# Kernel tuning notes

Measured on AMD Instinct MI355X. Metric: run time of the kernel, lower is better.

Reference implementation:

```python
import jax, jax.numpy as jnp
import numpy as np

QW_MAX = 127  # 2**(8-1) - 1


def setup_inputs() -> dict:
    key = jax.random.key(0)
    k1, k2, k3, k4, k5 = jax.random.split(key, 5)
    B, Din, H, Dout = 4096, 1024, 4096, 1024
    x = jax.random.normal(k1, (B, Din), dtype=jnp.float32)
    # float master weights (already transposed, as in quantify_weights: weight.T)
    w1f = jax.random.normal(k2, (Din, H), dtype=jnp.float32) * 0.02
    b1f = jax.random.normal(k3, (H,), dtype=jnp.float32) * 0.02
    w2f = jax.random.normal(k4, (H, Dout), dtype=jnp.float32) * 0.02
    b2f = jax.random.normal(k5, (Dout,), dtype=jnp.float32) * 0.02
    return {"x": x, "w1f": w1f, "b1f": b1f, "w2f": w2f, "b2f": b2f}


def _quantify_pair(w, b):
    # joint max-abs scale over weight and bias (matches quantify(x, x2))
    max_v = jnp.maximum(jnp.max(jnp.abs(w)), jnp.max(jnp.abs(b)))
    scale = max_v / QW_MAX
    wq = jnp.round(w / scale).astype(jnp.int8)
    bq = jnp.round(b / scale).astype(jnp.int8)
    return wq, bq, scale


def _dot_product(q_a, q_b, scale_a, scale_b, target_scale):
    # int8 GEMM with int32 accumulation, then requantize to int16
    y0 = q_a.astype(jnp.int32) @ q_b.astype(jnp.int32)  # [M, N] int32
    scale = scale_a * scale_b / target_scale
    return jnp.round(y0 * scale).astype(jnp.int16)


def reference(x, w1f, b1f, w2f, b2f):
    # weight quantization (done once at init in torch, inlined here)
    w1, b1, s1 = _quantify_pair(w1f, b1f)
    w2, b2, s2 = _quantify_pair(w2f, b2f)
    # dynamic activation quantization
    x_scale = jnp.max(jnp.abs(x)) / QW_MAX
    x_q = jnp.round(x / x_scale).astype(jnp.int8)
    # layer 1: target_scale = s1, so effective multiplier is x_scale
    o1 = _dot_product(x_q, w1, x_scale, s1, s1) + b1.astype(jnp.int16)
    # layer 2: note torch passes scale_1 (not x_scale) here — faithful to source
    o2 = _dot_product(jnp.maximum(o1, 0), w2, s1, s2, s2) + b2.astype(jnp.int16)
    # dequantize
    return o2.astype(jnp.float32) * s2
```

## Files before the change

kernel.cpp:

```cpp
#include <hip/hip_runtime.h>
#include <stdint.h>

typedef int   i32x4 __attribute__((ext_vector_type(4)));
typedef float f32x4 __attribute__((ext_vector_type(4)));

#define WS_PART    0
#define WS_XQ      32768
#define WS_W1QT    (WS_XQ   + 4096*1024)
#define WS_W2QT    (WS_W1QT + 4096*1024)
#define WS_PS      (WS_W2QT + 4096*1024)
#define WS_PH      (WS_PS   + 4096*4096)

__device__ __forceinline__ void async16(const void* g, void* l) {
  __builtin_amdgcn_global_load_lds(
      (const __attribute__((address_space(1))) unsigned*)g,
      (__attribute__((address_space(3))) unsigned*)l, 16, 0, 0);
}

__device__ __forceinline__ float block_absmax(const float* __restrict__ p0, int n0,
                                              const float* __restrict__ p1, int n1,
                                              float* red, float* slot) {
  int tid = threadIdx.x, nt = blockDim.x;
  float m = 0.f;
  for (int i = tid; i < n0; i += nt) m = fmaxf(m, fabsf(p0[i]));
  if (p1) for (int i = tid; i < n1; i += nt) m = fmaxf(m, fabsf(p1[i]));
  for (int off = 32; off; off >>= 1) m = fmaxf(m, __shfl_down(m, off));
  if ((tid & 63) == 0) red[tid >> 6] = m;
  __syncthreads();
  if (tid == 0) {
    int nw = nt >> 6;
    float M = red[0];
    for (int w = 1; w < nw; w++) M = fmaxf(M, red[w]);
    *slot = M;
  }
  __syncthreads();
  return *slot;
}

__global__ void k_absmax3(const float* __restrict__ x, const float* __restrict__ w1,
                          const float* __restrict__ w2, float* __restrict__ part) {
  int seg = blockIdx.x >> 9;
  int b = blockIdx.x & 511;
  const float* p = (seg == 0) ? x : (seg == 1) ? w1 : w2;
  int i = b * 256 + threadIdx.x;
  float m = 0.f;
  #pragma unroll
  for (int it = 0; it < 8; it++) {
    f32x4 v = ((const f32x4*)p)[i + it * 131072];
    m = fmaxf(m, fmaxf(fmaxf(fabsf(v.x), fabsf(v.y)), fmaxf(fabsf(v.z), fabsf(v.w))));
  }
  for (int off = 32; off; off >>= 1) m = fmaxf(m, __shfl_down(m, off));
  __shared__ float red[4];
  if ((threadIdx.x & 63) == 0) red[threadIdx.x >> 6] = m;
  __syncthreads();
  if (threadIdx.x == 0)
    part[blockIdx.x] = fmaxf(fmaxf(red[0], red[1]), fmaxf(red[2], red[3]));
}

__device__ __forceinline__ void quantT_body(const float* __restrict__ w, float s,
                                            i32x4* __restrict__ out, int C, int tkbits,
                                            int b) {
  int L = b * 256 + threadIdx.x;
  int h_in = L & 127;
  int kb = (L >> 7) & 3;
  int tk = (L >> 9) & ((1 << tkbits) - 1);
  int hblk = L >> (9 + tkbits);
  int h = hblk * 128 + h_in;
  int k0 = (tk * 4 + kb) * 16;
  int wd[4];
  #pragma unroll
  for (int d = 0; d < 4; d++) {
    unsigned acc = 0;
    #pragma unroll
    for (int j = 0; j < 4; j++) {
      float v = w[(size_t)(k0 + d * 4 + j) * C + h];
      int q = (int)rintf(v / s) & 255;
      acc |= (unsigned)q << (8 * j);
    }
    wd[d] = (int)acc;
  }
  i32x4 o; o.x = wd[0]; o.y = wd[1]; o.z = wd[2]; o.w = wd[3];
  out[L] = o;
}

__global__ void k_prep(const float* __restrict__ x, const float* __restrict__ w1f,
                       const float* __restrict__ w2f, const float* __restrict__ b1f,
                       const float* __restrict__ b2f, const float* __restrict__ part,
                       i32x4* __restrict__ xq, i32x4* __restrict__ w1qt,
                       i32x4* __restrict__ w2qt) {
  __shared__ float red[4];
  __shared__ float slot;
  int seg = blockIdx.x >> 10;
  int b = blockIdx.x & 1023;
  if (seg == 0) {
    float s = block_absmax(part, 512, nullptr, 0, red, &slot) / 127.0f;
    int L = b * 256 + threadIdx.x;
    int m_in = L & 127, kb = (L >> 7) & 3, tk = (L >> 9) & 15, mblk = L >> 13;
    int m = mblk * 128 + m_in;
    int k0 = (tk * 4 + kb) * 16;
    const f32x4* px = (const f32x4*)(x + m * 1024 + k0);
    int wd[4];
    #pragma unroll
    for (int d = 0; d < 4; d++) {
      f32x4 v = px[d];
      int b0 = (int)rintf(v.x / s) & 255;
      int b1 = (int)rintf(v.y / s) & 255;
      int b2 = (int)rintf(v.z / s) & 255;
      int b3 = (int)rintf(v.w / s) & 255;
      wd[d] = b0 | (b1 << 8) | (b2 << 16) | (b3 << 24);
    }
    i32x4 o; o.x = wd[0]; o.y = wd[1]; o.z = wd[2]; o.w = wd[3];
    xq[L] = o;
  } else if (seg == 1) {
    float s = block_absmax(part + 512, 512, b1f, 4096, red, &slot) / 127.0f;
    quantT_body(w1f, s, w1qt, 4096, 4, b);
  } else {
    float s = block_absmax(part + 1024, 512, b2f, 1024, red, &slot) / 127.0f;
    quantT_body(w2f, s, w2qt, 1024, 6, b);
  }
}

__launch_bounds__(256)
__global__ void k_gemm1(const i32x4* __restrict__ Aq, const i32x4* __restrict__ Bq,
                        const float* __restrict__ part, const float* __restrict__ b1f,
                        unsigned* __restrict__ plane_s, unsigned* __restrict__ plane_h) {
  __shared__ i32x4 As[2][512];
  __shared__ i32x4 Bs[2][512];
  __shared__ float red[4];
  __shared__ float slot;
  __shared__ int b1s[128];
  int tid = threadIdx.x;
  int bb = blockIdx.x;
  int hb = blockIdx.y;
  int lane = tid & 63, wid = tid >> 6;
  int wm = wid & 1, wn = wid >> 1;
  int g = lane >> 4, l15 = lane & 15;

  const i32x4* gA = Aq + (size_t)hb * 16 * 512;
  const i32x4* gB = Bq + (size_t)bb * 16 * 512;

  async16(gA + tid, &As[0][tid]);
  async16(gA + tid + 256, &As[0][tid + 256]);
  async16(gB + tid, &Bs[0][tid]);
  async16(gB + tid + 256, &Bs[0][tid + 256]);

  float sx  = block_absmax(part, 512, nullptr, 0, red, &slot) / 127.0f;
  float s1v = block_absmax(part + 512, 512, b1f, 4096, red, &slot) / 127.0f;
  float mult1 = sx * s1v / s1v;
  for (int i = tid; i < 128; i += 256)
    b1s[i] = (int)rintf(b1f[hb * 128 + i] / s1v);

  i32x4 acc[4][4];
  #pragma unroll
  for (int r = 0; r < 4; r++)
    #pragma unroll
    for (int c = 0; c < 4; c++) acc[r][c] = (i32x4)(0);

  int abase = g * 128 + wm * 64 + l15;
  int bbase = g * 128 + wn * 64 + l15;

  for (int t = 0; t < 16; ++t) {
    int cur = t & 1;
    __syncthreads();
    if (t + 1 < 16) {
      const i32x4* ga = gA + (t + 1) * 512;
      const i32x4* gb = gB + (t + 1) * 512;
      async16(ga + tid, &As[cur ^ 1][tid]);
      async16(ga + tid + 256, &As[cur ^ 1][tid + 256]);
      async16(gb + tid, &Bs[cur ^ 1][tid]);
      async16(gb + tid + 256, &Bs[cur ^ 1][tid + 256]);
    }
    i32x4 af[4], bf[4];
    #pragma unroll
    for (int r = 0; r < 4; r++) af[r] = As[cur][abase + r * 16];
    #pragma unroll
    for (int c = 0; c < 4; c++) bf[c] = Bs[cur][bbase + c * 16];
    #pragma unroll
    for (int r = 0; r < 4; r++)
      #pragma unroll
      for (int c = 0; c < 4; c++)
        acc[r][c] = __builtin_amdgcn_mfma_i32_16x16x64_i8(af[r], bf[c], acc[r][c], 0, 0, 0);
  }

  int t2base = hb * 2 + wm;
  #pragma unroll
  for (int r = 0; r < 4; r++) {
    int hloc = wm * 64 + r * 16 + 4 * g;
    int bq0 = b1s[hloc], bq1 = b1s[hloc + 1], bq2 = b1s[hloc + 2], bq3 = b1s[hloc + 3];
    #pragma unroll
    for (int c = 0; c < 4; c++) {
      unsigned lo = 0, hi = 0;
      #pragma unroll
      for (int q = 0; q < 4; q++) {
        int y0 = acc[r][c][q];
        int bqv = (q == 0) ? bq0 : (q == 1) ? bq1 : (q == 2) ? bq2 : bq3;
        int o = (short)((int)rintf((float)y0 * mult1) + bqv);
        int a = o > 0 ? o : 0;
        int s8 = (int)(signed char)(a & 0xFF);
        int h8 = (a >> 8) + (s8 < 0 ? 1 : 0);
        lo |= (unsigned)(s8 & 0xFF) << (8 * q);
        hi |= (unsigned)(h8 & 0xFF) << (8 * q);
      }
      int m_in = wn * 64 + c * 16 + l15;
      unsigned idx = (((unsigned)(bb * 64 + t2base) * 512u + (unsigned)(r * 128 + m_in)) << 2) + g;
      plane_s[idx] = lo;
      plane_h[idx] = hi;
    }
  }
}

__launch_bounds__(256)
__global__ void k_gemm2(const i32x4* __restrict__ Ps, const i32x4* __restrict__ Ph,
                        const i32x4* __restrict__ Bq, const float* __restrict__ part,
                        const float* __restrict__ b1f, const float* __restrict__ b2f,
                        float* __restrict__ out) {
  __shared__ i32x4 st[3][1024];
  __shared__ float red[4];
  __shared__ float slot;

  int tid = threadIdx.x;
  int bid = blockIdx.x;
  int wg  = (bid & 7) * 64 + (bid >> 3);
  int mb = wg >> 3;
  int nb = wg & 7;
  int mblk = mb >> 1, half = mb & 1;
  int wid = tid >> 6, lane = tid & 63;
  int wm = wid >> 1, wn = wid & 1;
  int g = lane >> 4, l15 = lane & 15;

  int a_src = wid * 128 + half * 64 + lane;
  int a_dst = wid * 64 + lane;

  #pragma unroll
  for (int tt = 0; tt < 2; ++tt) {
    const i32x4* pS = Ps + ((size_t)(mblk * 64 + tt) << 9);
    const i32x4* pH = Ph + ((size_t)(mblk * 64 + tt) << 9);
    const i32x4* pB = Bq + ((size_t)(nb * 64 + tt) << 9);
    async16(pS + a_src, &st[tt][a_dst]);
    async16(pH + a_src, &st[tt][256 + a_dst]);
    async16(pB + tid,       &st[tt][512 + tid]);
    async16(pB + tid + 256, &st[tt][768 + tid]);
  }

  float s1v = block_absmax(part + 512, 512, b1f, 4096, red, &slot) / 127.0f;
  float s2v = block_absmax(part + 1024, 512, b2f, 1024, red, &slot) / 127.0f;
  float mult2 = s1v * s2v / s2v;
  int bq4[4];
  #pragma unroll
  for (int c = 0; c < 4; c++)
    bq4[c] = (int)rintf(b2f[nb * 128 + wn * 64 + c * 16 + l15] / s2v);

  i32x4 accS[2][4], accH[2][4];
  #pragma unroll
  for (int r = 0; r < 2; r++)
    #pragma unroll
    for (int c = 0; c < 4; c++) { accS[r][c] = (i32x4)(0); accH[r][c] = (i32x4)(0); }

  int aoff = g * 64 + wm * 32 + l15;
  int boff = 512 + g * 128 + wn * 64 + l15;

  int cb = 0;
  for (int t = 0; t < 64; ++t) {
    if (t + 2 < 64) {
      int pb = cb + 2; if (pb >= 3) pb -= 3;
      const i32x4* pS = Ps + ((size_t)(mblk * 64 + t + 2) << 9);
      const i32x4* pH = Ph + ((size_t)(mblk * 64 + t + 2) << 9);
      const i32x4* pB = Bq + ((size_t)(nb * 64 + t + 2) << 9);
      async16(pS + a_src, &st[pb][a_dst]);
      async16(pH + a_src, &st[pb][256 + a_dst]);
      async16(pB + tid,       &st[pb][512 + tid]);
      async16(pB + tid + 256, &st[pb][768 + tid]);
    }
    i32x4 aS[2], aH[2], bf[4];
    #pragma unroll
    for (int r = 0; r < 2; r++) {
      aS[r] = st[cb][aoff + r * 16];
      aH[r] = st[cb][256 + aoff + r * 16];
    }
    #pragma unroll
    for (int c = 0; c < 4; c++) bf[c] = st[cb][boff + c * 16];
    __builtin_amdgcn_s_setprio(1);
    #pragma unroll
    for (int r = 0; r < 2; r++)
      #pragma unroll
      for (int c = 0; c < 4; c++) {
        accS[r][c] = __builtin_amdgcn_mfma_i32_16x16x64_i8(aS[r], bf[c], accS[r][c], 0, 0, 0);
        accH[r][c] = __builtin_amdgcn_mfma_i32_16x16x64_i8(aH[r], bf[c], accH[r][c], 0, 0, 0);
      }
    __builtin_amdgcn_s_setprio(0);
    if (t < 62) asm volatile("s_waitcnt vmcnt(4)");
    else        asm volatile("s_waitcnt vmcnt(0)");
    __builtin_amdgcn_s_barrier();
    __builtin_amdgcn_sched_barrier(0);
    cb = cb + 1; if (cb >= 3) cb -= 3;
  }

  #pragma unroll
  for (int r = 0; r < 2; r++) {
    int m0 = mb * 64 + wm * 32 + r * 16 + 4 * g;
    #pragma unroll
    for (int c = 0; c < 4; c++) {
      int n = nb * 128 + wn * 64 + c * 16 + l15;
      #pragma unroll
      for (int q = 0; q < 4; q++) {
        int y0 = accS[r][c][q] + accH[r][c][q] * 256;
        int o = (short)((int)rintf((float)y0 * mult2) + bq4[c]);
        out[(size_t)(m0 + q) * 1024 + n] = (float)o * s2v;
      }
    }
  }
}

extern "C" void kernel_launch(void* const* d_in, const int* in_sizes, int n_in,
                              void* d_out, int out_size, void* d_ws, size_t ws_size,
                              hipStream_t stream) {
  const float* x   = (const float*)d_in[0];
  const float* w1f = (const float*)d_in[1];
  const float* b1f = (const float*)d_in[2];
  const float* w2f = (const float*)d_in[3];
  const float* b2f = (const float*)d_in[4];
  float* out = (float*)d_out;

  char* ws = (char*)d_ws;
  float*  part    = (float*)(ws + WS_PART);
  i32x4*  xq      = (i32x4*)(ws + WS_XQ);
  i32x4*  w1qt    = (i32x4*)(ws + WS_W1QT);
  i32x4*  w2qt    = (i32x4*)(ws + WS_W2QT);
  unsigned* ps    = (unsigned*)(ws + WS_PS);
  unsigned* ph    = (unsigned*)(ws + WS_PH);

  k_absmax3<<<1536, 256, 0, stream>>>(x, w1f, w2f, part);
  k_prep<<<3072, 256, 0, stream>>>(x, w1f, w2f, b1f, b2f, part, xq, w1qt, w2qt);
  k_gemm1<<<dim3(32, 32), 256, 0, stream>>>(w1qt, xq, part, b1f, ps, ph);
  k_gemm2<<<512, 256, 0, stream>>>((const i32x4*)ps, (const i32x4*)ph, w2qt,
                                   part, b1f, b2f, out);
}
```

Before: 192.0 us.

## Split K across two wave groups in gemm2 with LDS reduction

```diff
diff --git a/kernel.cpp b/kernel.cpp
--- a/kernel.cpp
+++ b/kernel.cpp
@@ -209,46 +209,50 @@
   }
 }
 
-__launch_bounds__(256)
+__launch_bounds__(512, 4)
 __global__ void k_gemm2(const i32x4* __restrict__ Ps, const i32x4* __restrict__ Ph,
                         const i32x4* __restrict__ Bq, const float* __restrict__ part,
                         const float* __restrict__ b1f, const float* __restrict__ b2f,
                         float* __restrict__ out) {
-  __shared__ i32x4 st[3][1024];
-  __shared__ float red[4];
+  __shared__ i32x4 st[2048];
+  __shared__ float red[8];
   __shared__ float slot;
 
   int tid = threadIdx.x;
-  int bid = blockIdx.x;
-  int wg  = (bid & 7) * 64 + (bid >> 3);
-  int mb = wg >> 3;
-  int nb = wg & 7;
+  int L = blockIdx.x;
+  int mb = ((L & 7) << 3) | ((L >> 3) & 7);
+  int nb = L >> 6;
   int mblk = mb >> 1, half = mb & 1;
   int wid = tid >> 6, lane = tid & 63;
-  int wm = wid >> 1, wn = wid & 1;
+  int kh = wid >> 2, w2 = wid & 3;
+  int wm = w2 & 1, wn = w2 >> 1;
   int g = lane >> 4, l15 = lane & 15;
-
-  int a_src = wid * 128 + half * 64 + lane;
-  int a_dst = wid * 64 + lane;
-
-  #pragma unroll
-  for (int tt = 0; tt < 2; ++tt) {
-    const i32x4* pS = Ps + ((size_t)(mblk * 64 + tt) << 9);
-    const i32x4* pH = Ph + ((size_t)(mblk * 64 + tt) << 9);
-    const i32x4* pB = Bq + ((size_t)(nb * 64 + tt) << 9);
-    async16(pS + a_src, &st[tt][a_dst]);
-    async16(pH + a_src, &st[tt][256 + a_dst]);
-    async16(pB + tid,       &st[tt][512 + tid]);
-    async16(pB + tid + 256, &st[tt][768 + tid]);
+  int t256 = tid & 255;
+  int sbase = kh * 1024;
+  int a_idx = (t256 >> 6) * 128 + half * 64 + (t256 & 63);
+  int b_idx = g * 128 + wn * 64 + l15;
+
+  {
+    int t = kh * 32;
+    const i32x4* pS = Ps + ((size_t)(mblk * 64 + t) << 9);
+    const i32x4* pH = Ph + ((size_t)(mblk * 64 + t) << 9);
+    async16(pS + a_idx, &st[sbase + t256]);
+    async16(pH + a_idx, &st[sbase + 256 + t256]);
+  }
+  i32x4 bf[4];
+  {
+    const i32x4* pB = Bq + ((size_t)(nb * 64 + kh * 32) << 9);
+    #pragma unroll
+    for (int c = 0; c < 4; c++) bf[c] = pB[b_idx + c * 16];
   }
 
   float s1v = block_absmax(part + 512, 512, b1f, 4096, red, &slot) / 127.0f;
   float s2v = block_absmax(part + 1024, 512, b2f, 1024, red, &slot) / 127.0f;
   float mult2 = s1v * s2v / s2v;
-  int bq4[4];
+  int bq[4];
   #pragma unroll
   for (int c = 0; c < 4; c++)
-    bq4[c] = (int)rintf(b2f[nb * 128 + wn * 64 + c * 16 + l15] / s2v);
+    bq[c] = (int)rintf(b2f[nb * 128 + wn * 64 + c * 16 + l15] / s2v);
 
   i32x4 accS[2][4], accH[2][4];
   #pragma unroll
@@ -256,30 +260,24 @@
     #pragma unroll
     for (int c = 0; c < 4; c++) { accS[r][c] = (i32x4)(0); accH[r][c] = (i32x4)(0); }
 
-  int aoff = g * 64 + wm * 32 + l15;
-  int boff = 512 + g * 128 + wn * 64 + l15;
-
-  int cb = 0;
-  for (int t = 0; t < 64; ++t) {
-    if (t + 2 < 64) {
-      int pb = cb + 2; if (pb >= 3) pb -= 3;
-      const i32x4* pS = Ps + ((size_t)(mblk * 64 + t + 2) << 9);
-      const i32x4* pH = Ph + ((size_t)(mblk * 64 + t + 2) << 9);
-      const i32x4* pB = Bq + ((size_t)(nb * 64 + t + 2) << 9);
-      async16(pS + a_src, &st[pb][a_dst]);
-      async16(pH + a_src, &st[pb][256 + a_dst]);
-      async16(pB + tid,       &st[pb][512 + tid]);
-      async16(pB + tid + 256, &st[pb][768 + tid]);
-    }
-    i32x4 aS[2], aH[2], bf[4];
+  for (int tt = 0; tt < 32; ++tt) {
+    int cur = tt & 1;
+    __syncthreads();
+    if (tt + 1 < 32) {
+      int t = kh * 32 + tt + 1;
+      const i32x4* pS = Ps + ((size_t)(mblk * 64 + t) << 9);
+      const i32x4* pH = Ph + ((size_t)(mblk * 64 + t) << 9);
+      int R1 = sbase + (cur ^ 1) * 512;
+      async16(pS + a_idx, &st[R1 + t256]);
+      async16(pH + a_idx, &st[R1 + 256 + t256]);
+    }
+    int R = sbase + cur * 512;
+    i32x4 aS[2], aH[2];
     #pragma unroll
     for (int r = 0; r < 2; r++) {
-      aS[r] = st[cb][aoff + r * 16];
-      aH[r] = st[cb][256 + aoff + r * 16];
-    }
-    #pragma unroll
-    for (int c = 0; c < 4; c++) bf[c] = st[cb][boff + c * 16];
-    __builtin_amdgcn_s_setprio(1);
+      aS[r] = st[R + g * 64 + wm * 32 + r * 16 + l15];
+      aH[r] = st[R + 256 + g * 64 + wm * 32 + r * 16 + l15];
+    }
     #pragma unroll
     for (int r = 0; r < 2; r++)
       #pragma unroll
@@ -287,25 +285,47 @@
         accS[r][c] = __builtin_amdgcn_mfma_i32_16x16x64_i8(aS[r], bf[c], accS[r][c], 0, 0, 0);
         accH[r][c] = __builtin_amdgcn_mfma_i32_16x16x64_i8(aH[r], bf[c], accH[r][c], 0, 0, 0);
       }
-    __builtin_amdgcn_s_setprio(0);
-    if (t < 62) asm volatile("s_waitcnt vmcnt(4)");
-    else        asm volatile("s_waitcnt vmcnt(0)");
-    __builtin_amdgcn_s_barrier();
-    __builtin_amdgcn_sched_barrier(0);
-    cb = cb + 1; if (cb >= 3) cb -= 3;
-  }
-
-  #pragma unroll
-  for (int r = 0; r < 2; r++) {
-    int m0 = mb * 64 + wm * 32 + r * 16 + 4 * g;
-    #pragma unroll
-    for (int c = 0; c < 4; c++) {
-      int n = nb * 128 + wn * 64 + c * 16 + l15;
-      #pragma unroll
-      for (int q = 0; q < 4; q++) {
-        int y0 = accS[r][c][q] + accH[r][c][q] * 256;
-        int o = (short)((int)rintf((float)y0 * mult2) + bq4[c]);
-        out[(size_t)(m0 + q) * 1024 + n] = (float)o * s2v;
+    if (tt + 1 < 32) {
+      const i32x4* pB = Bq + ((size_t)(nb * 64 + kh * 32 + tt + 1) << 9);
+      #pragma unroll
+      for (int c = 0; c < 4; c++) bf[c] = pB[b_idx + c * 16];
+    }
+  }
+
+  int y0p[2][4][4];
+  #pragma unroll
+  for (int r = 0; r < 2; r++)
+    #pragma unroll
+    for (int c = 0; c < 4; c++)
+      #pragma unroll
+      for (int q = 0; q < 4; q++)
+        y0p[r][c][q] = accS[r][c][q] + accH[r][c][q] * 256;
+
+  __syncthreads();
+  int* mg = (int*)st;
+  if (kh == 1) {
+    #pragma unroll
+    for (int r = 0; r < 2; r++)
+      #pragma unroll
+      for (int c = 0; c < 4; c++)
+        #pragma unroll
+        for (int q = 0; q < 4; q++)
+          mg[((r * 4 + c) * 4 + q) * 256 + t256] = y0p[r][c][q];
+  }
+  __syncthreads();
+  if (kh == 0) {
+    #pragma unroll
+    for (int r = 0; r < 2; r++) {
+      int m0 = mb * 64 + wm * 32 + r * 16 + 4 * g;
+      #pragma unroll
+      for (int c = 0; c < 4; c++) {
+        int n = nb * 128 + wn * 64 + c * 16 + l15;
+        #pragma unroll
+        for (int q = 0; q < 4; q++) {
+          int y0 = y0p[r][c][q] + mg[((r * 4 + c) * 4 + q) * 256 + t256];
+          int o = (short)((int)rintf((float)y0 * mult2) + bq[c]);
+          out[(size_t)(m0 + q) * 1024 + n] = (float)o * s2v;
+        }
       }
     }
   }
@@ -332,6 +352,6 @@
   k_absmax3<<<1536, 256, 0, stream>>>(x, w1f, w2f, part);
   k_prep<<<3072, 256, 0, stream>>>(x, w1f, w2f, b1f, b2f, part, xq, w1qt, w2qt);
   k_gemm1<<<dim3(32, 32), 256, 0, stream>>>(w1qt, xq, part, b1f, ps, ph);
-  k_gemm2<<<512, 256, 0, stream>>>((const i32x4*)ps, (const i32x4*)ph, w2qt,
+  k_gemm2<<<512, 512, 0, stream>>>((const i32x4*)ps, (const i32x4*)ph, w2qt,
                                    part, b1f, b2f, out);
 }
```

After: 189.3 us. Within noise of the previous version (-1.4%).
